# Kernel optimization log

Hardware: AMD Instinct MI355X
Metric: run time of the kernel (lower is better)

Reference implementation:

```python
import jax, jax.numpy as jnp
import numpy as np

N = 3_000_000  # batch of deformation gradients


def setup_inputs() -> dict:
    key = jax.random.key(0)
    eye = jnp.eye(3, dtype=jnp.float32)
    noise = jax.random.normal(key, (N, 3, 3), dtype=jnp.float32)
    # near-identity deformation gradients so det(F) > 0 (log J well-defined)
    F = eye[None, :, :] + 0.05 * noise
    return {"F": F}


def _energy(F):
    """Strain energy density W(F) per sample. F: [N,3,3]."""
    g = jnp.array([4.0, 0.5, 0.5], dtype=F.dtype)  # transversely isotropic structural tensor (diagonal)
    C = jnp.einsum('nji,njk->nik', F, F)           # right Cauchy-Green C = F^T F, [N,3,3]
    I1 = jnp.trace(C, axis1=1, axis2=2)            # tr(C)
    J = jnp.linalg.det(F)                          # det(F)
    cofC = (J ** 2)[:, None, None] * jnp.linalg.inv(C)  # cof(C) = det(C) C^{-1}, det(C) = J^2
    I4 = jnp.einsum('nii,i->n', C, g)              # tr(C G), G diagonal
    I5 = jnp.einsum('nii,i->n', cofC, g)           # tr(cof(C) G)
    return 8.0 * I1 + 10.0 * J ** 2 - 56.0 * jnp.log(J) + 0.2 * (I4 ** 2 + I5 ** 2) - 44.0


def reference(F):
    # P = dW/dF, computed per sample; grad of the batch-sum gives per-sample grads
    return jax.grad(lambda f: jnp.sum(_energy(f)))(F)
```

## Files before the change

### kernel.cpp

```cpp
#include <hip/hip_runtime.h>


#define SAMPLES_PER_BLOCK 256
#define FLOATS_PER_BLOCK (SAMPLES_PER_BLOCK * 9)

__global__ __launch_bounds__(256) void pk1_grad_kernel(
    const float* __restrict__ Fin, float* __restrict__ Pout, int total_floats)
{
    __shared__ float lds[FLOATS_PER_BLOCK];
    const int t = threadIdx.x;
    const int base = blockIdx.x * FLOATS_PER_BLOCK;

#pragma unroll
    for (int i = 0; i < 9; ++i) {
        int g = base + i * 256 + t;
        lds[i * 256 + t] = (g < total_floats) ? Fin[g] : 1.0f;
    }
    __syncthreads();

    float f[9];
#pragma unroll
    for (int k = 0; k < 9; ++k) f[k] = lds[t * 9 + k];

    float c00 = f[4]*f[8] - f[5]*f[7];
    float c01 = f[5]*f[6] - f[3]*f[8];
    float c02 = f[3]*f[7] - f[4]*f[6];
    float c10 = f[2]*f[7] - f[1]*f[8];
    float c11 = f[0]*f[8] - f[2]*f[6];
    float c12 = f[1]*f[6] - f[0]*f[7];
    float c20 = f[1]*f[5] - f[2]*f[4];
    float c21 = f[2]*f[3] - f[0]*f[5];
    float c22 = f[0]*f[4] - f[1]*f[3];
    float J   = f[0]*c00 + f[1]*c01 + f[2]*c02;
    float invJ = 1.0f / J;

    float C00 = f[0]*f[0] + f[3]*f[3] + f[6]*f[6];
    float C11 = f[1]*f[1] + f[4]*f[4] + f[7]*f[7];
    float C22 = f[2]*f[2] + f[5]*f[5] + f[8]*f[8];
    float C01 = f[0]*f[1] + f[3]*f[4] + f[6]*f[7];
    float C02 = f[0]*f[2] + f[3]*f[5] + f[6]*f[8];
    float C12 = f[1]*f[2] + f[4]*f[5] + f[7]*f[8];

    float I4 = 4.0f*C00 + 0.5f*(C11 + C22);

    float K00 = C11*C22 - C12*C12;
    float K11 = C00*C22 - C02*C02;
    float K22 = C00*C11 - C01*C01;
    float K01 = C02*C12 - C01*C22;
    float K02 = C01*C12 - C02*C11;
    float K12 = C01*C02 - C00*C12;

    float I5 = 4.0f*K00 + 0.5f*(K11 + K22);

    float J2    = J * J;
    float alpha = (20.0f*J2 - 56.0f + 0.8f*I5*I5) * invJ;
    float beta  = 0.8f * I4;
    float gamma = -0.8f * I5 * invJ;

    float cf[3][3] = {{c00,c01,c02},{c10,c11,c12},{c20,c21,c22}};
    float K[3][3]  = {{K00,K01,K02},{K01,K11,K12},{K02,K12,K22}};
    const float g0 = 4.0f, g1 = 0.5f, g2 = 0.5f;
    const float gv[3] = {g0, g1, g2};

    float p[9];
#pragma unroll
    for (int i = 0; i < 3; ++i) {
        float a0 = cf[i][0] * g0;
        float a1 = cf[i][1] * g1;
        float a2 = cf[i][2] * g2;
#pragma unroll
        for (int j = 0; j < 3; ++j) {
            float M = a0 * K[0][j] + a1 * K[1][j] + a2 * K[2][j];
            p[3*i + j] = (16.0f + beta * gv[j]) * f[3*i + j]
                       + alpha * cf[i][j]
                       + gamma * M;
        }
    }

#pragma unroll
    for (int k = 0; k < 9; ++k) lds[t * 9 + k] = p[k];
    __syncthreads();

#pragma unroll
    for (int i = 0; i < 9; ++i) {
        int g = base + i * 256 + t;
        if (g < total_floats) Pout[g] = lds[i * 256 + t];
    }
}

extern "C" void kernel_launch(void* const* d_in, const int* in_sizes, int n_in,
                              void* d_out, int out_size, void* d_ws, size_t ws_size,
                              hipStream_t stream) {
    const float* F = (const float*)d_in[0];
    float* P = (float*)d_out;
    int total_floats = in_sizes[0];
    int blocks = (total_floats + FLOATS_PER_BLOCK - 1) / FLOATS_PER_BLOCK;
    pk1_grad_kernel<<<blocks, 256, 0, stream>>>(F, P, total_floats);
}
```

Baseline: 41.18 us.

## Vectorize to float2 loads/stores, two samples per thread, swizzled LDS, nontemporal stores

Switches global and LDS traffic to 8-byte float2 accesses and has each thread process two samples, so a block now covers 512 samples. An XOR swizzle on the LDS index is meant to reduce bank conflicts from the stride-9 per-thread reads and writes. Output goes through nontemporal stores, and launch bounds ask for higher occupancy. This raises register pressure, and it assumes the float count is even, which holds because N*9 with N even is even.

```diff
diff --git a/kernel.cpp b/kernel.cpp
--- a/kernel.cpp
+++ b/kernel.cpp
@@ -1,99 +1,126 @@
 #include <hip/hip_runtime.h>
 
 
-#define SAMPLES_PER_BLOCK 256
-#define FLOATS_PER_BLOCK (SAMPLES_PER_BLOCK * 9)
+typedef float f2 __attribute__((ext_vector_type(2)));
 
-__global__ __launch_bounds__(256) void pk1_grad_kernel(
-    const float* __restrict__ Fin, float* __restrict__ Pout, int total_floats)
+#define SAMPLES_PER_BLOCK 512
+#define F2_PER_BLOCK (SAMPLES_PER_BLOCK * 9 / 2)
+
+__device__ __forceinline__ int swz(int i) { return i ^ ((i >> 4) & 15); }
+
+__global__ __launch_bounds__(256, 8) void pk1_grad_kernel(
+    const f2* __restrict__ Fin, f2* __restrict__ Pout, int total2)
 {
-    __shared__ float lds[FLOATS_PER_BLOCK];
+    __shared__ f2 lds2[F2_PER_BLOCK];
     const int t = threadIdx.x;
-    const int base = blockIdx.x * FLOATS_PER_BLOCK;
+    const int base2 = blockIdx.x * F2_PER_BLOCK;
 
 #pragma unroll
-    for (int i = 0; i < 9; ++i) {
-        int g = base + i * 256 + t;
-        lds[i * 256 + t] = (g < total_floats) ? Fin[g] : 1.0f;
+    for (int j = 0; j < 9; ++j) {
+        int i = j * 256 + t;
+        int g = base2 + i;
+        f2 v;
+        if (g < total2) v = Fin[g];
+        else { v.x = 1.0f; v.y = 1.0f; }
+        lds2[swz(i)] = v;
     }
     __syncthreads();
 
-    float f[9];
+    float buf[18];
 #pragma unroll
-    for (int k = 0; k < 9; ++k) f[k] = lds[t * 9 + k];
+    for (int q = 0; q < 9; ++q) {
+        f2 v = lds2[swz(t * 9 + q)];
+        buf[2 * q]     = v.x;
+        buf[2 * q + 1] = v.y;
+    }
 
-    float c00 = f[4]*f[8] - f[5]*f[7];
-    float c01 = f[5]*f[6] - f[3]*f[8];
-    float c02 = f[3]*f[7] - f[4]*f[6];
-    float c10 = f[2]*f[7] - f[1]*f[8];
-    float c11 = f[0]*f[8] - f[2]*f[6];
-    float c12 = f[1]*f[6] - f[0]*f[7];
-    float c20 = f[1]*f[5] - f[2]*f[4];
-    float c21 = f[2]*f[3] - f[0]*f[5];
-    float c22 = f[0]*f[4] - f[1]*f[3];
-    float J   = f[0]*c00 + f[1]*c01 + f[2]*c02;
-    float invJ = 1.0f / J;
+#pragma unroll
+    for (int s = 0; s < 2; ++s) {
+        float f[9];
+#pragma unroll
+        for (int k = 0; k < 9; ++k) f[k] = buf[s * 9 + k];
 
-    float C00 = f[0]*f[0] + f[3]*f[3] + f[6]*f[6];
-    float C11 = f[1]*f[1] + f[4]*f[4] + f[7]*f[7];
-    float C22 = f[2]*f[2] + f[5]*f[5] + f[8]*f[8];
-    float C01 = f[0]*f[1] + f[3]*f[4] + f[6]*f[7];
-    float C02 = f[0]*f[2] + f[3]*f[5] + f[6]*f[8];
-    float C12 = f[1]*f[2] + f[4]*f[5] + f[7]*f[8];
+        float c00 = f[4]*f[8] - f[5]*f[7];
+        float c01 = f[5]*f[6] - f[3]*f[8];
+        float c02 = f[3]*f[7] - f[4]*f[6];
+        float c10 = f[2]*f[7] - f[1]*f[8];
+        float c11 = f[0]*f[8] - f[2]*f[6];
+        float c12 = f[1]*f[6] - f[0]*f[7];
+        float c20 = f[1]*f[5] - f[2]*f[4];
+        float c21 = f[2]*f[3] - f[0]*f[5];
+        float c22 = f[0]*f[4] - f[1]*f[3];
+        float J    = f[0]*c00 + f[1]*c01 + f[2]*c02;
+        float invJ = 1.0f / J;
 
-    float I4 = 4.0f*C00 + 0.5f*(C11 + C22);
+        float C00 = f[0]*f[0] + f[3]*f[3] + f[6]*f[6];
+        float C11 = f[1]*f[1] + f[4]*f[4] + f[7]*f[7];
+        float C22 = f[2]*f[2] + f[5]*f[5] + f[8]*f[8];
+        float C01 = f[0]*f[1] + f[3]*f[4] + f[6]*f[7];
+        float C02 = f[0]*f[2] + f[3]*f[5] + f[6]*f[8];
+        float C12 = f[1]*f[2] + f[4]*f[5] + f[7]*f[8];
 
-    float K00 = C11*C22 - C12*C12;
-    float K11 = C00*C22 - C02*C02;
-    float K22 = C00*C11 - C01*C01;
-    float K01 = C02*C12 - C01*C22;
-    float K02 = C01*C12 - C02*C11;
-    float K12 = C01*C02 - C00*C12;
+        float I4 = 4.0f*C00 + 0.5f*(C11 + C22);
 
-    float I5 = 4.0f*K00 + 0.5f*(K11 + K22);
+        float K00 = C11*C22 - C12*C12;
+        float K11 = C00*C22 - C02*C02;
+        float K22 = C00*C11 - C01*C01;
+        float K01 = C02*C12 - C01*C22;
+        float K02 = C01*C12 - C02*C11;
+        float K12 = C01*C02 - C00*C12;
 
-    float J2    = J * J;
-    float alpha = (20.0f*J2 - 56.0f + 0.8f*I5*I5) * invJ;
-    float beta  = 0.8f * I4;
-    float gamma = -0.8f * I5 * invJ;
+        float I5 = 4.0f*K00 + 0.5f*(K11 + K22);
 
-    float cf[3][3] = {{c00,c01,c02},{c10,c11,c12},{c20,c21,c22}};
-    float K[3][3]  = {{K00,K01,K02},{K01,K11,K12},{K02,K12,K22}};
-    const float g0 = 4.0f, g1 = 0.5f, g2 = 0.5f;
-    const float gv[3] = {g0, g1, g2};
+        float J2    = J * J;
+        float alpha = (20.0f*J2 - 56.0f + 0.8f*I5*I5) * invJ;
+        float beta  = 0.8f * I4;
+        float gamma = -0.8f * I5 * invJ;
 
-    float p[9];
+        float cf[3][3] = {{c00,c01,c02},{c10,c11,c12},{c20,c21,c22}};
+        float K[3][3]  = {{K00,K01,K02},{K01,K11,K12},{K02,K12,K22}};
+        const float gv[3] = {4.0f, 0.5f, 0.5f};
+
 #pragma unroll
-    for (int i = 0; i < 3; ++i) {
-        float a0 = cf[i][0] * g0;
-        float a1 = cf[i][1] * g1;
-        float a2 = cf[i][2] * g2;
+        for (int i = 0; i < 3; ++i) {
+            float a0 = cf[i][0] * 4.0f;
+            float a1 = cf[i][1] * 0.5f;
+            float a2 = cf[i][2] * 0.5f;
 #pragma unroll
-        for (int j = 0; j < 3; ++j) {
-            float M = a0 * K[0][j] + a1 * K[1][j] + a2 * K[2][j];
-            p[3*i + j] = (16.0f + beta * gv[j]) * f[3*i + j]
-                       + alpha * cf[i][j]
-                       + gamma * M;
+            for (int j = 0; j < 3; ++j) {
+                float M = a0 * K[0][j] + a1 * K[1][j] + a2 * K[2][j];
+                buf[s * 9 + 3 * i + j] =
+                      (16.0f + beta * gv[j]) * f[3 * i + j]
+                    + alpha * cf[i][j]
+                    + gamma * M;
+            }
         }
     }
 
 #pragma unroll
-    for (int k = 0; k < 9; ++k) lds[t * 9 + k] = p[k];
+    for (int q = 0; q < 9; ++q) {
+        f2 v;
+        v.x = buf[2 * q];
+        v.y = buf[2 * q + 1];
+        lds2[swz(t * 9 + q)] = v;
+    }
     __syncthreads();
 
 #pragma unroll
-    for (int i = 0; i < 9; ++i) {
-        int g = base + i * 256 + t;
-        if (g < total_floats) Pout[g] = lds[i * 256 + t];
+    for (int j = 0; j < 9; ++j) {
+        int i = j * 256 + t;
+        int g = base2 + i;
+        if (g < total2) {
+            f2 v = lds2[swz(i)];
+            __builtin_nontemporal_store(v, &Pout[g]);
+        }
     }
 }
 
 extern "C" void kernel_launch(void* const* d_in, const int* in_sizes, int n_in,
                               void* d_out, int out_size, void* d_ws, size_t ws_size,
                               hipStream_t stream) {
-    const float* F = (const float*)d_in[0];
-    float* P = (float*)d_out;
-    int total_floats = in_sizes[0];
-    int blocks = (total_floats + FLOATS_PER_BLOCK - 1) / FLOATS_PER_BLOCK;
-    pk1_grad_kernel<<<blocks, 256, 0, stream>>>(F, P, total_floats);
+    const f2* F = (const f2*)d_in[0];
+    f2* P = (f2*)d_out;
+    int total2 = in_sizes[0] / 2;
+    int blocks = (total2 + F2_PER_BLOCK - 1) / F2_PER_BLOCK;
+    pk1_grad_kernel<<<blocks, 256, 0, stream>>>(F, P, total2);
 }
```

New measurement: 121.0 us. +193.8%, slower.
